# Optimization experiments

Hardware: AMD Instinct MI355X
Metric: run time of the kernel (lower is better)

Reference implementation:

```python
import jax, jax.numpy as jnp
import numpy as np

G = 32               # sdf grid resolution (grid_size init default)
SCALE_FACTOR = 0.2   # forward default scale_factor
EPS = 1e-12


def setup_inputs() -> dict:
    key = jax.random.key(0)
    k1, k2 = jax.random.split(key)
    H, V, F = 2, 778, 1538  # two hands, MANO topology
    vertices = jax.random.normal(k1, (H, V, 3), dtype=jnp.float32)
    faces = jax.random.randint(k2, (F, 3), 0, V, dtype=jnp.int32)
    return {"vertices": vertices, "faces": faces}


def _sdiv(n, d):
    return n / jnp.where(jnp.abs(d) < EPS, EPS, d)


def _point_tri_dist2(p, a, b, c):
    # p: [P,1,3]; a,b,c: [1,F,3] -> squared distance [P,F] (Ericson closest-point)
    ab = b - a; ac = c - a; ap = p - a
    d1 = jnp.sum(ab * ap, -1); d2 = jnp.sum(ac * ap, -1)
    bp = p - b; d3 = jnp.sum(ab * bp, -1); d4 = jnp.sum(ac * bp, -1)
    cp = p - c; d5 = jnp.sum(ab * cp, -1); d6 = jnp.sum(ac * cp, -1)
    vc = d1 * d4 - d3 * d2
    vb = d5 * d2 - d1 * d6
    va = d3 * d6 - d5 * d4
    denom = va + vb + vc
    v_in = _sdiv(vb, denom); w_in = _sdiv(vc, denom)
    res = a + ab * v_in[..., None] + ac * w_in[..., None]  # face interior
    # edge BC
    cond = ((va <= 0) & ((d4 - d3) >= 0) & ((d5 - d6) >= 0))[..., None]
    w = _sdiv(d4 - d3, (d4 - d3) + (d5 - d6))[..., None]
    res = jnp.where(cond, b + (c - b) * w, res)
    # edge AC
    cond = ((vb <= 0) & (d2 >= 0) & (d6 <= 0))[..., None]
    w = _sdiv(d2, d2 - d6)[..., None]
    res = jnp.where(cond, a + ac * w, res)
    # edge AB
    cond = ((vc <= 0) & (d1 >= 0) & (d3 <= 0))[..., None]
    w = _sdiv(d1, d1 - d3)[..., None]
    res = jnp.where(cond, a + ab * w, res)
    # vertex regions (highest precedence)
    res = jnp.where(((d6 >= 0) & (d5 <= d6))[..., None], jnp.broadcast_to(c, res.shape), res)
    res = jnp.where(((d3 >= 0) & (d4 <= d3))[..., None], jnp.broadcast_to(b, res.shape), res)
    res = jnp.where(((d1 <= 0) & (d2 <= 0))[..., None], jnp.broadcast_to(a, res.shape), res)
    return jnp.sum((p - res) ** 2, -1)


def _inside(p, a, b, c):
    # parity of +x ray intersections (Moller-Trumbore with dir = (1,0,0))
    e1 = b - a; e2 = c - a
    det = e1[..., 1] * (-e2[..., 2]) + e1[..., 2] * e2[..., 1]  # dot(e1, cross(dir,e2))
    inv = _sdiv(1.0, det)
    s = p - a
    u = (s[..., 1] * (-e2[..., 2]) + s[..., 2] * e2[..., 1]) * inv
    q = jnp.cross(s, e1)
    v = q[..., 0] * inv                # dot(dir, q)
    t = jnp.sum(e2 * q, -1) * inv
    hit = (jnp.abs(det) > 1e-9) & (u >= 0) & (u <= 1) & (v >= 0) & (u + v <= 1) & (t > 0)
    return (jnp.sum(hit.astype(jnp.int32), axis=-1) % 2) == 1


def _sdf_grid(tri):
    # tri: [F,3,3] scaled triangles -> phi [G,G,G] laid out [z,y,x] (grid_sample DHW)
    a = tri[None, :, 0]; b = tri[None, :, 1]; c = tri[None, :, 2]
    lin = jnp.linspace(-1.0, 1.0, G, dtype=tri.dtype)
    zz, yy, xx = jnp.meshgrid(lin, lin, lin, indexing='ij')
    pts = jnp.stack([xx, yy, zz], -1).reshape(G, G * G, 3)  # chunk over z-slabs

    def slab(ps):
        p = ps[:, None, :]
        d2 = jnp.min(_point_tri_dist2(p, a, b, c), axis=1)
        ins = _inside(p, a, b, c)
        return jnp.where(ins, jnp.sqrt(jnp.maximum(d2, 0.0)), 0.0)

    return jax.lax.map(slab, pts).reshape(G, G, G)


def _trilinear(phi, coords):
    # grid_sample(align_corners=True, padding_mode='zeros'), coords [N,3] in xyz order
    g = G - 1
    f = (coords + 1.0) * 0.5 * g
    fx, fy, fz = f[:, 0], f[:, 1], f[:, 2]
    x0f = jnp.floor(fx); y0f = jnp.floor(fy); z0f = jnp.floor(fz)
    wx = fx - x0f; wy = fy - y0f; wz = fz - z0f
    x0 = x0f.astype(jnp.int32); y0 = y0f.astype(jnp.int32); z0 = z0f.astype(jnp.int32)

    def corner(zi, yi, xi, w):
        valid = (zi >= 0) & (zi <= g) & (yi >= 0) & (yi <= g) & (xi >= 0) & (xi <= g)
        val = phi[jnp.clip(zi, 0, g), jnp.clip(yi, 0, g), jnp.clip(xi, 0, g)]
        return jnp.where(valid, val, 0.0) * w

    out = (corner(z0, y0, x0, (1 - wz) * (1 - wy) * (1 - wx))
           + corner(z0, y0, x0 + 1, (1 - wz) * (1 - wy) * wx)
           + corner(z0, y0 + 1, x0, (1 - wz) * wy * (1 - wx))
           + corner(z0, y0 + 1, x0 + 1, (1 - wz) * wy * wx)
           + corner(z0 + 1, y0, x0, wz * (1 - wy) * (1 - wx))
           + corner(z0 + 1, y0, x0 + 1, wz * (1 - wy) * wx)
           + corner(z0 + 1, y0 + 1, x0, wz * wy * (1 - wx))
           + corner(z0 + 1, y0 + 1, x0 + 1, wz * wy * wx))
    return out


def reference(vertices, faces):
    H = vertices.shape[0]
    bmin = vertices.min(axis=1)   # [H,3]
    bmax = vertices.max(axis=1)
    center = jax.lax.stop_gradient(((bmin + bmax) * 0.5)[:, None, :])           # [H,1,3]
    scale = jax.lax.stop_gradient(
        ((1.0 + SCALE_FACTOR) * 0.5 * (bmax - bmin).max(-1))[:, None, None])    # [H,1,1]
    v_scaled = jax.lax.stop_gradient((vertices - center) / scale)
    tris = v_scaled[:, faces]                                                    # [H,F,3,3]
    phi = jax.lax.stop_gradient(jax.vmap(_sdf_grid)(tris))                       # [H,G,G,G]
    i = 1  # hardcoded loop 'for i in [1]' in the source
    coords = ((vertices - center[i][None]) / scale[i][None]).reshape(-1, 3)
    phi_val = _trilinear(phi[i], coords).reshape(H, -1)
    weights = jnp.ones((H, 1), dtype=vertices.dtype).at[i, 0].set(0.0)
    loss = jnp.sum(weights * phi_val) / (H ** 2)
    return loss
```

## Files before the change

### kernel.cpp

```cpp
#include <hip/hip_runtime.h>
#include <math.h>

#define NNODE 32768
#define NTHR  256
#define CH    192

__device__ __forceinline__ float rguard(float d) {
    float dd = (fabsf(d) < 1e-12f) ? 1e-12f : d;
    return __builtin_amdgcn_rcpf(dd);
}

__device__ __forceinline__ void cell_of(float px, float py, float pz,
                                        int& x0, int& y0, int& z0,
                                        float& wx, float& wy, float& wz) {
#pragma clang fp contract(off)
    float fx = (px + 1.0f) * 0.5f * 31.0f;
    float fy = (py + 1.0f) * 0.5f * 31.0f;
    float fz = (pz + 1.0f) * 0.5f * 31.0f;
    float x0f = floorf(fx), y0f = floorf(fy), z0f = floorf(fz);
    wx = fx - x0f; wy = fy - y0f; wz = fz - z0f;
    x0 = (int)fmaxf(fminf(x0f, 33.0f), -2.0f);
    y0 = (int)fmaxf(fminf(y0f, 33.0f), -2.0f);
    z0 = (int)fmaxf(fminf(z0f, 33.0f), -2.0f);
}

__device__ __forceinline__ void bbox_of(const float* __restrict__ verts, int V,
                                        float& ocx, float& ocy, float& ocz,
                                        float& osc) {
#pragma clang fp contract(off)
    const float* v1 = verts + (size_t)V * 3;
    float mn[3] = {1e30f, 1e30f, 1e30f};
    float mx[3] = {-1e30f, -1e30f, -1e30f};
    for (int i = threadIdx.x; i < V; i += blockDim.x) {
        for (int c = 0; c < 3; ++c) {
            float val = v1[i * 3 + c];
            mn[c] = fminf(mn[c], val);
            mx[c] = fmaxf(mx[c], val);
        }
    }
    for (int off = 32; off >= 1; off >>= 1) {
        for (int c = 0; c < 3; ++c) {
            mn[c] = fminf(mn[c], __shfl_down(mn[c], off));
            mx[c] = fmaxf(mx[c], __shfl_down(mx[c], off));
        }
    }
    __shared__ float smn[16][3], smx[16][3];
    int wv = threadIdx.x >> 6, lane = threadIdx.x & 63;
    if (lane == 0)
        for (int c = 0; c < 3; ++c) { smn[wv][c] = mn[c]; smx[wv][c] = mx[c]; }
    __syncthreads();
    const int nw = (int)blockDim.x >> 6;
    float ext = -1e30f, cc[3];
    for (int c = 0; c < 3; ++c) {
        float lo = 1e30f, hi = -1e30f;
        for (int w = 0; w < nw; ++w) {
            lo = fminf(lo, smn[w][c]);
            hi = fmaxf(hi, smx[w][c]);
        }
        cc[c] = (lo + hi) * 0.5f;
        ext = fmaxf(ext, hi - lo);
    }
    ocx = cc[0]; ocy = cc[1]; ocz = cc[2];
    osc = (1.0f + 0.2f) * 0.5f * ext;
    __syncthreads();
}

__device__ __forceinline__ void tri_node(
        float ax, float ay, float az, float abx, float aby, float abz,
        float acx, float acy, float acz, float inv, float det,
        float dbb, float dbc, float dcc,
        float px, float py, float pz, float& mind2, int& h) {
    float apx = px - ax, apy = py - ay, apz = pz - az;
    {
#pragma clang fp contract(fast)
        float d1 = abx * apx + aby * apy + abz * apz;
        float d2 = acx * apx + acy * apy + acz * apz;
        float d3 = d1 - dbb;
        float d4 = d2 - dbc;
        float d5 = d1 - dbc;
        float d6 = d2 - dcc;
        float vc = d1 * d4 - d3 * d2;
        float vb = d5 * d2 - d1 * d6;
        float va = d3 * d6 - d5 * d4;
        float denom = va + vb + vc;
        float rd = rguard(denom);
        float v_in = vb * rd, w_in = vc * rd;
        float rx = ax + abx * v_in + acx * w_in;
        float ry = ay + aby * v_in + acy * w_in;
        float rz = az + abz * v_in + acz * w_in;
        if (va <= 0.0f && (d4 - d3) >= 0.0f && (d5 - d6) >= 0.0f) {
            float w2 = (d4 - d3) * rguard((d4 - d3) + (d5 - d6));
            rx = ax + abx + (acx - abx) * w2;
            ry = ay + aby + (acy - aby) * w2;
            rz = az + abz + (acz - abz) * w2;
        }
        if (vb <= 0.0f && d2 >= 0.0f && d6 <= 0.0f) {
            float w2 = d2 * rguard(d2 - d6);
            rx = ax + acx * w2; ry = ay + acy * w2; rz = az + acz * w2;
        }
        if (vc <= 0.0f && d1 >= 0.0f && d3 <= 0.0f) {
            float w2 = d1 * rguard(d1 - d3);
            rx = ax + abx * w2; ry = ay + aby * w2; rz = az + abz * w2;
        }
        if (d6 >= 0.0f && d5 <= d6) { rx = ax + acx; ry = ay + acy; rz = az + acz; }
        if (d3 >= 0.0f && d4 <= d3) { rx = ax + abx; ry = ay + aby; rz = az + abz; }
        if (d1 <= 0.0f && d2 <= 0.0f) { rx = ax; ry = ay; rz = az; }
        float ddx = px - rx, ddy = py - ry, ddz = pz - rz;
        mind2 = fminf(mind2, ddx * ddx + ddy * ddy + ddz * ddz);
    }
    {
#pragma clang fp contract(off)
        float u = (apy * (-acz) + apz * acy) * inv;
        float qx = apy * abz - apz * aby;
        float qy = apz * abx - apx * abz;
        float qz = apx * aby - apy * abx;
        float v = qx * inv;
        float tt = (acx * qx + acy * qy + acz * qz) * inv;
        h += (fabsf(det) > 1e-9f && u >= 0.0f && u <= 1.0f && v >= 0.0f &&
              (u + v) <= 1.0f && tt > 0.0f) ? 1 : 0;
    }
}

__global__ void __launch_bounds__(NTHR) k_setup(
        const float* __restrict__ verts, const int* __restrict__ faces,
        float* __restrict__ tri, unsigned int* __restrict__ d2b,
        int* __restrict__ hits, int* __restrict__ cnt, int* __restrict__ list,
        int V, int F) {
    float cx0, cy0, cz0, sc;
    bbox_of(verts, V, cx0, cy0, cz0, sc);
    const int b = (int)blockIdx.x, tid = threadIdx.x;

    for (int t = b * NTHR + tid; t < NNODE; t += (int)gridDim.x * NTHR) {
        d2b[t] = 0xFFFFFFFFu;
        hits[t] = 0;
    }

    if (b == 0) {
        __shared__ unsigned bm[NNODE / 32];
        __shared__ int scnt[NTHR];
        for (int k = 0; k < 4; ++k) bm[tid * 4 + k] = 0u;
        __syncthreads();
        for (int i = tid; i < V; i += NTHR) {
#pragma clang fp contract(off)
            float px = (verts[i * 3 + 0] - cx0) / sc;
            float py = (verts[i * 3 + 1] - cy0) / sc;
            float pz = (verts[i * 3 + 2] - cz0) / sc;
            int x0, y0, z0; float wx, wy, wz;
            cell_of(px, py, pz, x0, y0, z0, wx, wy, wz);
            for (int k = 0; k < 8; ++k) {
                int zi = z0 + ((k >> 2) & 1), yi = y0 + ((k >> 1) & 1),
                    xi = x0 + (k & 1);
                if ((unsigned)zi < 32u && (unsigned)yi < 32u && (unsigned)xi < 32u) {
                    int node = (zi * 32 + yi) * 32 + xi;
                    atomicOr(&bm[node >> 5], 1u << (node & 31));
                }
            }
        }
        __syncthreads();
        unsigned w0 = bm[tid * 4 + 0], w1 = bm[tid * 4 + 1],
                 w2 = bm[tid * 4 + 2], w3 = bm[tid * 4 + 3];
        int c = __popc(w0) + __popc(w1) + __popc(w2) + __popc(w3);
        scnt[tid] = c;
        __syncthreads();
        for (int off = 1; off < NTHR; off <<= 1) {
            int v_ = (tid >= off) ? scnt[tid - off] : 0;
            __syncthreads();
            scnt[tid] += v_;
            __syncthreads();
        }
        if (tid == NTHR - 1) cnt[0] = scnt[NTHR - 1];
        int off = scnt[tid] - c;
        unsigned wsv[4] = {w0, w1, w2, w3};
        for (int k = 0; k < 4; ++k) {
            unsigned w = wsv[k];
            int basebit = (tid * 4 + k) * 32;
            while (w) {
                int bb = __ffs(w) - 1;
                list[off++] = basebit + bb;
                w &= w - 1;
            }
        }
    } else {
        int f = (b - 1) * NTHR + tid;
        if (f < F) {
#pragma clang fp contract(off)
            const float* v1 = verts + (size_t)V * 3;
            int i0 = faces[f * 3 + 0], i1 = faces[f * 3 + 1], i2 = faces[f * 3 + 2];
            float ax = (v1[i0 * 3 + 0] - cx0) / sc, ay = (v1[i0 * 3 + 1] - cy0) / sc,
                  az = (v1[i0 * 3 + 2] - cz0) / sc;
            float bx = (v1[i1 * 3 + 0] - cx0) / sc, by = (v1[i1 * 3 + 1] - cy0) / sc,
                  bz = (v1[i1 * 3 + 2] - cz0) / sc;
            float cx = (v1[i2 * 3 + 0] - cx0) / sc, cy = (v1[i2 * 3 + 1] - cy0) / sc,
                  cz = (v1[i2 * 3 + 2] - cz0) / sc;
            float abx = bx - ax, aby = by - ay, abz = bz - az;
            float acx = cx - ax, acy = cy - ay, acz = cz - az;
            float det = aby * (-acz) + abz * acy;
            float dd = (fabsf(det) < 1e-12f) ? 1e-12f : det;
            float inv = 1.0f / dd;
            float* r = tri + (size_t)f * 16;
            r[0] = ax;  r[1] = ay;  r[2] = az;
            r[3] = abx; r[4] = aby; r[5] = abz;
            r[6] = acx; r[7] = acy; r[8] = acz;
            r[9] = inv; r[10] = det;
            r[11] = abx * abx + aby * aby + abz * abz;
            r[12] = abx * acx + aby * acy + abz * acz;
            r[13] = acx * acx + acy * acy + acz * acz;
            r[14] = 0.0f; r[15] = 0.0f;
        }
    }
}

__global__ void __launch_bounds__(NTHR) k_main(
        const float* __restrict__ tri, const int* __restrict__ list,
        const int* __restrict__ cnt, unsigned int* __restrict__ d2b,
        int* __restrict__ hits, int F, int nch) {
    const int n = cnt[0];
    const int group = (int)blockIdx.x / nch;
    if (group * 4 >= n) return;
    const int c = (int)blockIdx.x - group * nch;
    const int cbase = c * CH;
    const int tn = min(CH, F - cbase);

    __shared__ float s[14][CH];
    const int tid = threadIdx.x, lane = tid & 63;
    for (int j = tid; j < tn; j += NTHR) {
        const float4* g = (const float4*)(tri + (size_t)(cbase + j) * 16);
        float4 r0 = g[0], r1 = g[1], r2 = g[2], r3 = g[3];
        s[0][j] = r0.x;  s[1][j] = r0.y;  s[2][j] = r0.z;  s[3][j] = r0.w;
        s[4][j] = r1.x;  s[5][j] = r1.y;  s[6][j] = r1.z;  s[7][j] = r1.w;
        s[8][j] = r2.x;  s[9][j] = r2.y;  s[10][j] = r2.z; s[11][j] = r2.w;
        s[12][j] = r3.x; s[13][j] = r3.y;
    }
    __syncthreads();

    const int idx = group * 4 + (tid >> 6);
    const int node = (idx < n) ? list[idx] : -1;
    float px = 0, py = 0, pz = 0;
    if (node >= 0) {
#pragma clang fp contract(off)
        px = (float)((double)(node & 31) * (2.0 / 31.0) - 1.0);
        py = (float)((double)((node >> 5) & 31) * (2.0 / 31.0) - 1.0);
        pz = (float)((double)(node >> 10) * (2.0 / 31.0) - 1.0);
    }
    float m = 1e30f;
    int h = 0;
    if (node >= 0) {
        for (int mi = 0; mi * 64 < tn; ++mi) {
            int j = lane + mi * 64;
            if (j < tn) {
                tri_node(s[0][j], s[1][j], s[2][j], s[3][j], s[4][j], s[5][j],
                         s[6][j], s[7][j], s[8][j], s[9][j], s[10][j],
                         s[11][j], s[12][j], s[13][j], px, py, pz, m, h);
            }
        }
    }
    for (int off = 32; off >= 1; off >>= 1) {
        m = fminf(m, __shfl_xor(m, off));
        h += __shfl_xor(h, off);
    }
    if (lane == 0 && node >= 0) {
        atomicMin(d2b + node, __float_as_uint(m));
        atomicAdd(hits + node, h);
    }
}

__global__ void k_sum(const float* __restrict__ verts,
                      const unsigned int* __restrict__ d2b, const int* __restrict__ hits,
                      float* __restrict__ out, int V) {
    float cx, cy, cz, sc;
    bbox_of(verts, V, cx, cy, cz, sc);
    {
#pragma clang fp contract(off)
        __shared__ float sm[1024];
        const int tid = threadIdx.x;
        float val = 0.0f;
        for (int i = tid; i < V; i += 1024) {
            float px = (verts[i * 3 + 0] - cx) / sc;
            float py = (verts[i * 3 + 1] - cy) / sc;
            float pz = (verts[i * 3 + 2] - cz) / sc;
            int x0, y0, z0; float wx, wy, wz;
            cell_of(px, py, pz, x0, y0, z0, wx, wy, wz);
            auto corner = [&](int zi, int yi, int xi, float w) -> float {
#pragma clang fp contract(off)
                bool valid = (zi >= 0) && (zi <= 31) && (yi >= 0) && (yi <= 31) &&
                             (xi >= 0) && (xi <= 31);
                int zc = min(max(zi, 0), 31);
                int yc = min(max(yi, 0), 31);
                int xc = min(max(xi, 0), 31);
                int idx = (zc * 32 + yc) * 32 + xc;
                float vv = (hits[idx] & 1)
                               ? sqrtf(fmaxf(__uint_as_float(d2b[idx]), 0.0f))
                               : 0.0f;
                return valid ? vv * w : 0.0f;
            };
            val += corner(z0, y0, x0, (1.0f - wz) * (1.0f - wy) * (1.0f - wx))
                 + corner(z0, y0, x0 + 1, (1.0f - wz) * (1.0f - wy) * wx)
                 + corner(z0, y0 + 1, x0, (1.0f - wz) * wy * (1.0f - wx))
                 + corner(z0, y0 + 1, x0 + 1, (1.0f - wz) * wy * wx)
                 + corner(z0 + 1, y0, x0, wz * (1.0f - wy) * (1.0f - wx))
                 + corner(z0 + 1, y0, x0 + 1, wz * (1.0f - wy) * wx)
                 + corner(z0 + 1, y0 + 1, x0, wz * wy * (1.0f - wx))
                 + corner(z0 + 1, y0 + 1, x0 + 1, wz * wy * wx);
        }
        sm[tid] = val;
        __syncthreads();
        for (int ss = 512; ss >= 1; ss >>= 1) {
            if (tid < ss) sm[tid] += sm[tid + ss];
            __syncthreads();
        }
        if (tid == 0) out[0] = sm[0] * 0.25f;
    }
}

extern "C" void kernel_launch(void* const* d_in, const int* in_sizes, int n_in,
                              void* d_out, int out_size, void* d_ws, size_t ws_size,
                              hipStream_t stream) {
    const float* verts = (const float*)d_in[0];
    const int* faces = (const int*)d_in[1];
    float* out = (float*)d_out;
    float* ws = (float*)d_ws;

    int V = in_sizes[0] / 6;
    int F = in_sizes[1] / 3;

    float* tri = ws;
    unsigned int* d2b = (unsigned int*)(tri + 16 * (size_t)F);
    int* hits = (int*)(d2b + NNODE);
    int* cnt = hits + NNODE;
    int* list = cnt + 1;

    int nrec = (F + NTHR - 1) / NTHR;
    int nch = (F + CH - 1) / CH;
    int nmax = 8 * V; if (nmax > NNODE) nmax = NNODE;
    int nblk_main = ((nmax + 3) / 4) * nch;

    k_setup<<<1 + nrec, NTHR, 0, stream>>>(verts, faces, tri, d2b, hits, cnt, list,
                                           V, F);
    k_main<<<nblk_main, NTHR, 0, stream>>>(tri, list, cnt, d2b, hits, F, nch);
    k_sum<<<1, 1024, 0, stream>>>(verts, d2b, hits, out, V);
}
```

Before: 45.45 us.

## Fuse final sum into main kernel via last-block counter and enlarge face chunks

Folds the trilinear-sum kernel into k_main. A global completion counter lets the last finishing block do the final reduction, which removes one kernel launch. The face chunk size also grows from 192 to 256, and a small remainder is merged into the last chunk (up to 319 faces), so fewer blocks each load more work into shared memory. The risks are atomic traffic on the counter from every block, a single 256-thread block doing the tail reduction instead of 1024 threads, and relaxed memory ordering when reading the other blocks' results.

New measurement: 140.1 us. +208.3%, slower.

```diff
diff --git a/kernel.cpp b/kernel.cpp
--- a/kernel.cpp
+++ b/kernel.cpp
@@ -3,7 +3,8 @@
 
 #define NNODE 32768
 #define NTHR  256
-#define CH    192
+#define CH    256
+#define MAXC  (CH + 63)
 
 __device__ __forceinline__ float rguard(float d) {
     float dd = (fabsf(d) < 1e-12f) ? 1e-12f : d;
@@ -124,8 +125,8 @@
 __global__ void __launch_bounds__(NTHR) k_setup(
         const float* __restrict__ verts, const int* __restrict__ faces,
         float* __restrict__ tri, unsigned int* __restrict__ d2b,
-        int* __restrict__ hits, int* __restrict__ cnt, int* __restrict__ list,
-        int V, int F) {
+        int* __restrict__ hits, int* __restrict__ cnt, int* __restrict__ done,
+        int* __restrict__ list, int V, int F) {
     float cx0, cy0, cz0, sc;
     bbox_of(verts, V, cx0, cy0, cz0, sc);
     const int b = (int)blockIdx.x, tid = threadIdx.x;
@@ -134,6 +135,7 @@
         d2b[t] = 0xFFFFFFFFu;
         hits[t] = 0;
     }
+    if (b == 0 && tid == 0) done[0] = 0;
 
     if (b == 0) {
         __shared__ unsigned bm[NNODE / 32];
@@ -213,68 +215,75 @@
 __global__ void __launch_bounds__(NTHR) k_main(
         const float* __restrict__ tri, const int* __restrict__ list,
         const int* __restrict__ cnt, unsigned int* __restrict__ d2b,
-        int* __restrict__ hits, int F, int nch) {
+        int* __restrict__ hits, int* __restrict__ done,
+        const float* __restrict__ verts, float* __restrict__ out,
+        int F, int nch, int V) {
     const int n = cnt[0];
     const int group = (int)blockIdx.x / nch;
-    if (group * 4 >= n) return;
-    const int c = (int)blockIdx.x - group * nch;
-    const int cbase = c * CH;
-    const int tn = min(CH, F - cbase);
-
-    __shared__ float s[14][CH];
     const int tid = threadIdx.x, lane = tid & 63;
-    for (int j = tid; j < tn; j += NTHR) {
-        const float4* g = (const float4*)(tri + (size_t)(cbase + j) * 16);
-        float4 r0 = g[0], r1 = g[1], r2 = g[2], r3 = g[3];
-        s[0][j] = r0.x;  s[1][j] = r0.y;  s[2][j] = r0.z;  s[3][j] = r0.w;
-        s[4][j] = r1.x;  s[5][j] = r1.y;  s[6][j] = r1.z;  s[7][j] = r1.w;
-        s[8][j] = r2.x;  s[9][j] = r2.y;  s[10][j] = r2.z; s[11][j] = r2.w;
-        s[12][j] = r3.x; s[13][j] = r3.y;
-    }
+    const bool active = (group * 4 < n);
+
+    if (active) {
+        const int c = (int)blockIdx.x - group * nch;
+        const int cbase = c * CH;
+        const int tn = (c == nch - 1) ? (F - cbase) : CH;
+
+        __shared__ float s[14][MAXC];
+        for (int j = tid; j < tn; j += NTHR) {
+            const float4* g = (const float4*)(tri + (size_t)(cbase + j) * 16);
+            float4 r0 = g[0], r1 = g[1], r2 = g[2], r3 = g[3];
+            s[0][j] = r0.x;  s[1][j] = r0.y;  s[2][j] = r0.z;  s[3][j] = r0.w;
+            s[4][j] = r1.x;  s[5][j] = r1.y;  s[6][j] = r1.z;  s[7][j] = r1.w;
+            s[8][j] = r2.x;  s[9][j] = r2.y;  s[10][j] = r2.z; s[11][j] = r2.w;
+            s[12][j] = r3.x; s[13][j] = r3.y;
+        }
+        __syncthreads();
+
+        const int idx = group * 4 + (tid >> 6);
+        const int node = (idx < n) ? list[idx] : -1;
+        float px = 0, py = 0, pz = 0;
+        if (node >= 0) {
+#pragma clang fp contract(off)
+            px = (float)((double)(node & 31) * (2.0 / 31.0) - 1.0);
+            py = (float)((double)((node >> 5) & 31) * (2.0 / 31.0) - 1.0);
+            pz = (float)((double)(node >> 10) * (2.0 / 31.0) - 1.0);
+        }
+        float m = 1e30f;
+        int h = 0;
+        if (node >= 0) {
+            for (int mi = 0; mi * 64 < tn; ++mi) {
+                int j = lane + mi * 64;
+                if (j < tn) {
+                    tri_node(s[0][j], s[1][j], s[2][j], s[3][j], s[4][j], s[5][j],
+                             s[6][j], s[7][j], s[8][j], s[9][j], s[10][j],
+                             s[11][j], s[12][j], s[13][j], px, py, pz, m, h);
+                }
+            }
+        }
+        for (int off = 32; off >= 1; off >>= 1) {
+            m = fminf(m, __shfl_xor(m, off));
+            h += __shfl_xor(h, off);
+        }
+        if (lane == 0 && node >= 0) {
+            atomicMin(d2b + node, __float_as_uint(m));
+            atomicAdd(hits + node, h);
+        }
+    }
+
+    __shared__ int lastflag;
     __syncthreads();
-
-    const int idx = group * 4 + (tid >> 6);
-    const int node = (idx < n) ? list[idx] : -1;
-    float px = 0, py = 0, pz = 0;
-    if (node >= 0) {
-#pragma clang fp contract(off)
-        px = (float)((double)(node & 31) * (2.0 / 31.0) - 1.0);
-        py = (float)((double)((node >> 5) & 31) * (2.0 / 31.0) - 1.0);
-        pz = (float)((double)(node >> 10) * (2.0 / 31.0) - 1.0);
-    }
-    float m = 1e30f;
-    int h = 0;
-    if (node >= 0) {
-        for (int mi = 0; mi * 64 < tn; ++mi) {
-            int j = lane + mi * 64;
-            if (j < tn) {
-                tri_node(s[0][j], s[1][j], s[2][j], s[3][j], s[4][j], s[5][j],
-                         s[6][j], s[7][j], s[8][j], s[9][j], s[10][j],
-                         s[11][j], s[12][j], s[13][j], px, py, pz, m, h);
-            }
-        }
-    }
-    for (int off = 32; off >= 1; off >>= 1) {
-        m = fminf(m, __shfl_xor(m, off));
-        h += __shfl_xor(h, off);
-    }
-    if (lane == 0 && node >= 0) {
-        atomicMin(d2b + node, __float_as_uint(m));
-        atomicAdd(hits + node, h);
-    }
-}
-
-__global__ void k_sum(const float* __restrict__ verts,
-                      const unsigned int* __restrict__ d2b, const int* __restrict__ hits,
-                      float* __restrict__ out, int V) {
+    if (tid == 0)
+        lastflag = (atomicAdd(done, 1) == (int)gridDim.x - 1) ? 1 : 0;
+    __syncthreads();
+    if (!lastflag) return;
+
     float cx, cy, cz, sc;
     bbox_of(verts, V, cx, cy, cz, sc);
     {
 #pragma clang fp contract(off)
-        __shared__ float sm[1024];
-        const int tid = threadIdx.x;
+        __shared__ float sm[NTHR];
         float val = 0.0f;
-        for (int i = tid; i < V; i += 1024) {
+        for (int i = tid; i < V; i += NTHR) {
             float px = (verts[i * 3 + 0] - cx) / sc;
             float py = (verts[i * 3 + 1] - cy) / sc;
             float pz = (verts[i * 3 + 2] - cz) / sc;
@@ -288,9 +297,12 @@
                 int yc = min(max(yi, 0), 31);
                 int xc = min(max(xi, 0), 31);
                 int idx = (zc * 32 + yc) * 32 + xc;
-                float vv = (hits[idx] & 1)
-                               ? sqrtf(fmaxf(__uint_as_float(d2b[idx]), 0.0f))
-                               : 0.0f;
+                unsigned dbits = __hip_atomic_load(&d2b[idx], __ATOMIC_RELAXED,
+                                                   __HIP_MEMORY_SCOPE_AGENT);
+                int hh = __hip_atomic_load(&hits[idx], __ATOMIC_RELAXED,
+                                           __HIP_MEMORY_SCOPE_AGENT);
+                float vv = (hh & 1) ? sqrtf(fmaxf(__uint_as_float(dbits), 0.0f))
+                                    : 0.0f;
                 return valid ? vv * w : 0.0f;
             };
             val += corner(z0, y0, x0, (1.0f - wz) * (1.0f - wy) * (1.0f - wx))
@@ -304,7 +316,7 @@
         }
         sm[tid] = val;
         __syncthreads();
-        for (int ss = 512; ss >= 1; ss >>= 1) {
+        for (int ss = NTHR / 2; ss >= 1; ss >>= 1) {
             if (tid < ss) sm[tid] += sm[tid + ss];
             __syncthreads();
         }
@@ -327,15 +339,20 @@
     unsigned int* d2b = (unsigned int*)(tri + 16 * (size_t)F);
     int* hits = (int*)(d2b + NNODE);
     int* cnt = hits + NNODE;
-    int* list = cnt + 1;
+    int* done = cnt + 1;
+    int* list = done + 1;
 
     int nrec = (F + NTHR - 1) / NTHR;
-    int nch = (F + CH - 1) / CH;
+    int nch = F / CH;
+    int rem = F - nch * CH;
+    if (nch == 0 || rem >= 64) nch += (rem > 0 ? 1 : 0);
+    if (nch == 0) nch = 1;
+
     int nmax = 8 * V; if (nmax > NNODE) nmax = NNODE;
     int nblk_main = ((nmax + 3) / 4) * nch;
 
-    k_setup<<<1 + nrec, NTHR, 0, stream>>>(verts, faces, tri, d2b, hits, cnt, list,
-                                           V, F);
-    k_main<<<nblk_main, NTHR, 0, stream>>>(tri, list, cnt, d2b, hits, F, nch);
-    k_sum<<<1, 1024, 0, stream>>>(verts, d2b, hits, out, V);
-}
+    k_setup<<<1 + nrec, NTHR, 0, stream>>>(verts, faces, tri, d2b, hits, cnt, done,
+                                           list, V, F);
+    k_main<<<nblk_main, NTHR, 0, stream>>>(tri, list, cnt, d2b, hits, done, verts,
+                                           out, F, nch, V);
+}
```
